# Kernel optimization log

Hardware: AMD Instinct MI355X
Metric: run time of the kernel (lower is better)

Reference implementation:

```python
import jax, jax.numpy as jnp
import numpy as np

TEMPERATURE = 0.05
EPS = 1e-8  # F.cosine_similarity default eps


def setup_inputs() -> dict:
    key = jax.random.key(0)
    k1, k2 = jax.random.split(key)
    N, D = 8192, 256
    return {
        "query_embeddings": jax.random.normal(k1, (N, D), dtype=jnp.float32),
        "pos_embeddings": jax.random.normal(k2, (N, D), dtype=jnp.float32),
    }


def _normalize(x):
    # matches F.cosine_similarity: x / max(||x||, eps)
    norm = jnp.sqrt(jnp.sum(x * x, axis=-1, keepdims=True))
    return x / jnp.maximum(norm, EPS)


def reference(query_embeddings, pos_embeddings):
    q = _normalize(query_embeddings)  # [N, D]
    p = _normalize(pos_embeddings)    # [N, D]
    # cosine similarity matrix via GEMM instead of (N,N,D) broadcast
    sim = jnp.einsum("nd,md->nm", q, p) / TEMPERATURE  # [N, N]
    # cross-entropy with labels = arange(N): loss_i = logsumexp(sim_i) - sim_ii
    logz = jax.nn.logsumexp(sim, axis=-1)  # [N]
    diag = jnp.diagonal(sim)               # [N]
    loss = jnp.mean(logz - diag)
    return loss
```

## Files before the change

kernel.cpp:

```cpp
#include <hip/hip_runtime.h>
#include <hip/hip_bf16.h>

#define NROWS 8192
#define DDIM  256
#define INV_TEMP 20.0f

typedef __attribute__((ext_vector_type(8))) short bf16x8;
typedef __attribute__((ext_vector_type(4))) float f32x4;

__device__ static inline void async16(const void* g, void* l) {
    __builtin_amdgcn_global_load_lds(
        (const __attribute__((address_space(1))) void*)g,
        (__attribute__((address_space(3))) void*)l, 16, 0, 0);
}

__global__ __launch_bounds__(256) void norm_diag_kernel(
    const float* __restrict__ q, const float* __restrict__ p,
    unsigned short* __restrict__ qn, unsigned short* __restrict__ pn,
    float* __restrict__ diag, int* __restrict__ tickets)
{
    if (blockIdx.x == 0 && threadIdx.x == 0) tickets[0] = 0;

    const int row  = (blockIdx.x << 2) + (threadIdx.x >> 6);
    const int lane = threadIdx.x & 63;

    const float4 qv = ((const float4*)(q + (size_t)row * DDIM))[lane];
    const float4 pv = ((const float4*)(p + (size_t)row * DDIM))[lane];

    float sq = qv.x*qv.x + qv.y*qv.y + qv.z*qv.z + qv.w*qv.w;
    float sp = pv.x*pv.x + pv.y*pv.y + pv.z*pv.z + pv.w*pv.w;
    #pragma unroll
    for (int m = 1; m < 64; m <<= 1) {
        sq += __shfl_xor(sq, m);
        sp += __shfl_xor(sp, m);
    }
    const float qs = 1.0f / fmaxf(sqrtf(sq), 1e-8f);
    const float ps = 1.0f / fmaxf(sqrtf(sp), 1e-8f);

    const float qx = qv.x*qs, qy = qv.y*qs, qz = qv.z*qs, qw = qv.w*qs;
    const float px = pv.x*ps, py = pv.y*ps, pz = pv.z*ps, pw = pv.w*ps;

    float d = qx*px + qy*py + qz*pz + qw*pw;
    #pragma unroll
    for (int m = 1; m < 64; m <<= 1) d += __shfl_xor(d, m);
    if (lane == 0) diag[row] = d * INV_TEMP;

    union { unsigned short u16[4]; uint2 v; } uq, up;
    {
        __hip_bfloat16 b;
        b = __float2bfloat16(qx); uq.u16[0] = *(unsigned short*)&b;
        b = __float2bfloat16(qy); uq.u16[1] = *(unsigned short*)&b;
        b = __float2bfloat16(qz); uq.u16[2] = *(unsigned short*)&b;
        b = __float2bfloat16(qw); uq.u16[3] = *(unsigned short*)&b;
        b = __float2bfloat16(px); up.u16[0] = *(unsigned short*)&b;
        b = __float2bfloat16(py); up.u16[1] = *(unsigned short*)&b;
        b = __float2bfloat16(pz); up.u16[2] = *(unsigned short*)&b;
        b = __float2bfloat16(pw); up.u16[3] = *(unsigned short*)&b;
    }
    *(uint2*)(qn + (size_t)row * DDIM + lane * 4) = uq.v;
    *(uint2*)(pn + (size_t)row * DDIM + lane * 4) = up.v;
}

__global__ __launch_bounds__(512, 2) void simexp_kernel(
    const unsigned short* __restrict__ qn,
    const unsigned short* __restrict__ pn,
    float* __restrict__ part)
{
    __shared__ unsigned char lds[3 * 32768];

    const int tid  = threadIdx.x;
    const int lane = tid & 63;
    const int w    = tid >> 6;
    const int wr   = w >> 2;
    const int wc   = w & 3;
    const int quad = lane >> 4;
    const int l16  = lane & 15;

    const int L   = blockIdx.y * 32 + blockIdx.x;
    const int xcd = L & 7;
    const int c   = L >> 3;
    const int rowblk = xcd * 4 + (c & 3);
    const int colblk = c >> 2;
    const int rowbase = rowblk * 256;
    const int colbase = colblk * 256;

    const unsigned short* gA0 = qn + (size_t)(rowbase + (2*w  )*16 + l16) * DDIM + quad * 8;
    const unsigned short* gA1 = qn + (size_t)(rowbase + (2*w+1)*16 + l16) * DDIM + quad * 8;
    const unsigned short* gB0 = pn + (size_t)(colbase + (2*w  )*16 + l16) * DDIM + quad * 8;
    const unsigned short* gB1 = pn + (size_t)(colbase + (2*w+1)*16 + l16) * DDIM + quad * 8;

    f32x4 acc[8][4];
    #pragma unroll
    for (int i = 0; i < 8; ++i)
        #pragma unroll
        for (int j = 0; j < 4; ++j) acc[i][j] = (f32x4)0.0f;

#define STAGE(buf, ks) do {                                             \
        unsigned char* _b = lds + (buf) * 32768;                        \
        async16(gA0 + (ks) * 32, _b +         (2*w    ) * 1024);        \
        async16(gA1 + (ks) * 32, _b +         (2*w + 1) * 1024);        \
        async16(gB0 + (ks) * 32, _b + 16384 + (2*w    ) * 1024);        \
        async16(gB1 + (ks) * 32, _b + 16384 + (2*w + 1) * 1024);        \
    } while (0)

    STAGE(0, 0);
    STAGE(1, 1);
    asm volatile("s_waitcnt vmcnt(4)" ::: "memory");
    __builtin_amdgcn_s_barrier();
    asm volatile("" ::: "memory");

    #pragma unroll
    for (int ks = 0; ks < 8; ++ks) {
        if (ks < 6) STAGE((ks + 2) % 3, ks + 2);

        const unsigned char* ba = lds + (ks % 3) * 32768;
        bf16x8 af[8], bf[4];
        #pragma unroll
        for (int i = 0; i < 8; ++i)
            af[i] = *(const bf16x8*)(ba + (wr*8 + i) * 1024 + quad * 256 + l16 * 16);
        #pragma unroll
        for (int j = 0; j < 4; ++j)
            bf[j] = *(const bf16x8*)(ba + 16384 + (wc*4 + j) * 1024 + quad * 256 + l16 * 16);

        #pragma unroll
        for (int i = 0; i < 8; ++i)
            #pragma unroll
            for (int j = 0; j < 4; ++j)
                acc[i][j] = __builtin_amdgcn_mfma_f32_16x16x32_bf16(
                    af[i], bf[j], acc[i][j], 0, 0, 0);

        if (ks < 7) {
            if (ks < 6) { asm volatile("s_waitcnt vmcnt(4)" ::: "memory"); }
            else        { asm volatile("s_waitcnt vmcnt(0)" ::: "memory"); }
            __builtin_amdgcn_s_barrier();
            asm volatile("" ::: "memory");
        }
    }
#undef STAGE

    __syncthreads();
    float* red = (float*)lds;

    #pragma unroll
    for (int i = 0; i < 8; ++i)
        #pragma unroll
        for (int r = 0; r < 4; ++r) {
            float s = __expf(acc[i][0][r] * INV_TEMP)
                    + __expf(acc[i][1][r] * INV_TEMP)
                    + __expf(acc[i][2][r] * INV_TEMP)
                    + __expf(acc[i][3][r] * INV_TEMP);
            s += __shfl_xor(s, 1);
            s += __shfl_xor(s, 2);
            s += __shfl_xor(s, 4);
            s += __shfl_xor(s, 8);
            if (l16 == 0)
                red[wc * 256 + wr * 128 + i * 16 + quad * 4 + r] = s;
        }
    __syncthreads();

    if (tid < 256)
        part[(size_t)colblk * NROWS + rowbase + tid] =
            red[tid] + red[256 + tid] + red[512 + tid] + red[768 + tid];
}

__global__ __launch_bounds__(128) void rowsum_final_kernel(
    const float* __restrict__ part, const float* __restrict__ diag,
    float* __restrict__ loss_part, int* __restrict__ tickets,
    float* __restrict__ out)
{
    const int row = blockIdx.x * 128 + threadIdx.x;
    float s = 0.0f;
    #pragma unroll 4
    for (int cb = 0; cb < 32; ++cb)
        s += part[(size_t)cb * NROWS + row];
    float v = logf(s) - diag[row];

    #pragma unroll
    for (int m = 1; m < 64; m <<= 1) v += __shfl_xor(v, m);
    __shared__ float wsum[2];
    __shared__ int swin;
    if ((threadIdx.x & 63) == 0) wsum[threadIdx.x >> 6] = v;
    __syncthreads();
    if (threadIdx.x == 0) {
        __hip_atomic_store(&loss_part[blockIdx.x], wsum[0] + wsum[1],
            __ATOMIC_RELEASE, __HIP_MEMORY_SCOPE_AGENT);
        swin = __hip_atomic_fetch_add(&tickets[0], 1,
                   __ATOMIC_ACQ_REL, __HIP_MEMORY_SCOPE_AGENT);
    }
    __syncthreads();
    if (swin != 63) return;

    if (threadIdx.x < 64) {
        float x = __hip_atomic_load(&loss_part[threadIdx.x],
                      __ATOMIC_RELAXED, __HIP_MEMORY_SCOPE_AGENT);
        #pragma unroll
        for (int m = 1; m < 64; m <<= 1) x += __shfl_xor(x, m);
        if (threadIdx.x == 0) out[0] = x * (1.0f / NROWS);
    }
}

extern "C" void kernel_launch(void* const* d_in, const int* in_sizes, int n_in,
                              void* d_out, int out_size, void* d_ws, size_t ws_size,
                              hipStream_t stream)
{
    const float* q = (const float*)d_in[0];
    const float* p = (const float*)d_in[1];

    char* ws = (char*)d_ws;
    unsigned short* qn   = (unsigned short*)ws;
    unsigned short* pn   = (unsigned short*)(ws + (size_t)NROWS*DDIM*2);
    float* part      = (float*)(ws + 2*(size_t)NROWS*DDIM*2);
    float* diag      = part + 32 * (size_t)NROWS;
    float* loss_part = diag + NROWS;
    int*   tickets   = (int*)(loss_part + 64);

    norm_diag_kernel<<<NROWS/4, 256, 0, stream>>>(q, p, qn, pn, diag, tickets);

    dim3 grid(32, 32);
    simexp_kernel<<<grid, 512, 0, stream>>>(qn, pn, part);

    rowsum_final_kernel<<<64, 128, 0, stream>>>(part, diag, loss_part,
                                                tickets, (float*)d_out);
}
```

Before: 131.1 us.

## Shrink GEMM tile to 256x128 with 4-wave-per-SIMD occupancy and 64 column partials

Changes the similarity GEMM tile from 256x256 to 256x128, halving per-wave accumulators (4x4 MFMA tiles) and LDS per buffer so four 512-thread blocks can be resident per CU. The grid doubles to 2048 blocks with a 1D launch, and each wave now issues three async loads per stage instead of four. The row-sum kernel reads 64 column-block partials instead of 32. The aim is better latency hiding through higher occupancy, paid for with lower arithmetic intensity per tile and extra global partial traffic.

```diff
diff --git a/kernel.cpp b/kernel.cpp
--- a/kernel.cpp
+++ b/kernel.cpp
@@ -61,51 +61,62 @@
     *(uint2*)(pn + (size_t)row * DDIM + lane * 4) = up.v;
 }
 
-__global__ __launch_bounds__(512, 2) void simexp_kernel(
+__global__ __launch_bounds__(512, 4) void simexp_kernel(
     const unsigned short* __restrict__ qn,
     const unsigned short* __restrict__ pn,
     float* __restrict__ part)
 {
-    __shared__ unsigned char lds[3 * 32768];
+    __shared__ unsigned char lds[3 * 24576];
 
     const int tid  = threadIdx.x;
     const int lane = tid & 63;
     const int w    = tid >> 6;
-    const int wr   = w >> 2;
-    const int wc   = w & 3;
+    const int wr   = w >> 1;
+    const int wc   = w & 1;
     const int quad = lane >> 4;
     const int l16  = lane & 15;
-
-    const int L   = blockIdx.y * 32 + blockIdx.x;
+    const int loff = lane * 16;
+
+    const int L   = blockIdx.x;
     const int xcd = L & 7;
     const int c   = L >> 3;
     const int rowblk = xcd * 4 + (c & 3);
     const int colblk = c >> 2;
     const int rowbase = rowblk * 256;
-    const int colbase = colblk * 256;
-
-    const unsigned short* gA0 = qn + (size_t)(rowbase + (2*w  )*16 + l16) * DDIM + quad * 8;
-    const unsigned short* gA1 = qn + (size_t)(rowbase + (2*w+1)*16 + l16) * DDIM + quad * 8;
-    const unsigned short* gB0 = pn + (size_t)(colbase + (2*w  )*16 + l16) * DDIM + quad * 8;
-    const unsigned short* gB1 = pn + (size_t)(colbase + (2*w+1)*16 + l16) * DDIM + quad * 8;
-
-    f32x4 acc[8][4];
-    #pragma unroll
-    for (int i = 0; i < 8; ++i)
+    const int colbase = colblk * 128;
+
+    const unsigned short* gsrc0; const unsigned short* gsrc1;
+    const unsigned short* gsrc2;
+    int ldst0, ldst1, ldst2;
+    {
+        const int i0 = 3*w, i1 = 3*w + 1, i2 = 3*w + 2;
+        gsrc0 = (i0 < 16) ? qn + (size_t)(rowbase + i0*16 + l16) * DDIM + quad * 8
+                          : pn + (size_t)(colbase + (i0-16)*16 + l16) * DDIM + quad * 8;
+        ldst0 = (i0 < 16) ? i0 * 1024 : 16384 + (i0-16) * 1024;
+        gsrc1 = (i1 < 16) ? qn + (size_t)(rowbase + i1*16 + l16) * DDIM + quad * 8
+                          : pn + (size_t)(colbase + (i1-16)*16 + l16) * DDIM + quad * 8;
+        ldst1 = (i1 < 16) ? i1 * 1024 : 16384 + (i1-16) * 1024;
+        gsrc2 = (i2 < 16) ? qn + (size_t)(rowbase + i2*16 + l16) * DDIM + quad * 8
+                          : pn + (size_t)(colbase + (i2-16)*16 + l16) * DDIM + quad * 8;
+        ldst2 = (i2 < 16) ? i2 * 1024 : 16384 + (i2-16) * 1024;
+    }
+
+    f32x4 acc[4][4];
+    #pragma unroll
+    for (int i = 0; i < 4; ++i)
         #pragma unroll
         for (int j = 0; j < 4; ++j) acc[i][j] = (f32x4)0.0f;
 
 #define STAGE(buf, ks) do {                                             \
-        unsigned char* _b = lds + (buf) * 32768;                        \
-        async16(gA0 + (ks) * 32, _b +         (2*w    ) * 1024);        \
-        async16(gA1 + (ks) * 32, _b +         (2*w + 1) * 1024);        \
-        async16(gB0 + (ks) * 32, _b + 16384 + (2*w    ) * 1024);        \
-        async16(gB1 + (ks) * 32, _b + 16384 + (2*w + 1) * 1024);        \
+        unsigned char* _b = lds + (buf) * 24576;                        \
+        async16(gsrc0 + (ks) * 32, _b + ldst0);                         \
+        async16(gsrc1 + (ks) * 32, _b + ldst1);                         \
+        async16(gsrc2 + (ks) * 32, _b + ldst2);                         \
     } while (0)
 
     STAGE(0, 0);
     STAGE(1, 1);
-    asm volatile("s_waitcnt vmcnt(4)" ::: "memory");
+    asm volatile("s_waitcnt vmcnt(3)" ::: "memory");
     __builtin_amdgcn_s_barrier();
     asm volatile("" ::: "memory");
 
@@ -113,24 +124,24 @@
     for (int ks = 0; ks < 8; ++ks) {
         if (ks < 6) STAGE((ks + 2) % 3, ks + 2);
 
-        const unsigned char* ba = lds + (ks % 3) * 32768;
-        bf16x8 af[8], bf[4];
-        #pragma unroll
-        for (int i = 0; i < 8; ++i)
-            af[i] = *(const bf16x8*)(ba + (wr*8 + i) * 1024 + quad * 256 + l16 * 16);
+        const unsigned char* ba = lds + (ks % 3) * 24576;
+        bf16x8 af[4], bf[4];
+        #pragma unroll
+        for (int i = 0; i < 4; ++i)
+            af[i] = *(const bf16x8*)(ba + (wr*4 + i) * 1024 + loff);
         #pragma unroll
         for (int j = 0; j < 4; ++j)
-            bf[j] = *(const bf16x8*)(ba + 16384 + (wc*4 + j) * 1024 + quad * 256 + l16 * 16);
-
-        #pragma unroll
-        for (int i = 0; i < 8; ++i)
+            bf[j] = *(const bf16x8*)(ba + 16384 + (wc*4 + j) * 1024 + loff);
+
+        #pragma unroll
+        for (int i = 0; i < 4; ++i)
             #pragma unroll
             for (int j = 0; j < 4; ++j)
                 acc[i][j] = __builtin_amdgcn_mfma_f32_16x16x32_bf16(
                     af[i], bf[j], acc[i][j], 0, 0, 0);
 
         if (ks < 7) {
-            if (ks < 6) { asm volatile("s_waitcnt vmcnt(4)" ::: "memory"); }
+            if (ks < 6) { asm volatile("s_waitcnt vmcnt(3)" ::: "memory"); }
             else        { asm volatile("s_waitcnt vmcnt(0)" ::: "memory"); }
             __builtin_amdgcn_s_barrier();
             asm volatile("" ::: "memory");
@@ -142,7 +153,7 @@
     float* red = (float*)lds;
 
     #pragma unroll
-    for (int i = 0; i < 8; ++i)
+    for (int i = 0; i < 4; ++i)
         #pragma unroll
         for (int r = 0; r < 4; ++r) {
             float s = __expf(acc[i][0][r] * INV_TEMP)
@@ -154,13 +165,12 @@
             s += __shfl_xor(s, 4);
             s += __shfl_xor(s, 8);
             if (l16 == 0)
-                red[wc * 256 + wr * 128 + i * 16 + quad * 4 + r] = s;
+                red[wc * 256 + wr * 64 + i * 16 + quad * 4 + r] = s;
         }
     __syncthreads();
 
     if (tid < 256)
-        part[(size_t)colblk * NROWS + rowbase + tid] =
-            red[tid] + red[256 + tid] + red[512 + tid] + red[768 + tid];
+        part[(size_t)colblk * NROWS + rowbase + tid] = red[tid] + red[256 + tid];
 }
 
 __global__ __launch_bounds__(128) void rowsum_final_kernel(
@@ -171,7 +181,7 @@
     const int row = blockIdx.x * 128 + threadIdx.x;
     float s = 0.0f;
     #pragma unroll 4
-    for (int cb = 0; cb < 32; ++cb)
+    for (int cb = 0; cb < 64; ++cb)
         s += part[(size_t)cb * NROWS + row];
     float v = logf(s) - diag[row];
 
@@ -210,14 +220,13 @@
     unsigned short* qn   = (unsigned short*)ws;
     unsigned short* pn   = (unsigned short*)(ws + (size_t)NROWS*DDIM*2);
     float* part      = (float*)(ws + 2*(size_t)NROWS*DDIM*2);
-    float* diag      = part + 32 * (size_t)NROWS;
+    float* diag      = part + 64 * (size_t)NROWS;
     float* loss_part = diag + NROWS;
     int*   tickets   = (int*)(loss_part + 64);
 
     norm_diag_kernel<<<NROWS/4, 256, 0, stream>>>(q, p, qn, pn, diag, tickets);
 
-    dim3 grid(32, 32);
-    simexp_kernel<<<grid, 512, 0, stream>>>(qn, pn, part);
+    simexp_kernel<<<2048, 512, 0, stream>>>(qn, pn, part);
 
     rowsum_final_kernel<<<64, 128, 0, stream>>>(part, diag, loss_part,
                                                 tickets, (float*)d_out);
```

New measurement: 124.2 us (median of 2 runs). -5.3%, faster.
